# Optimization experiments

Hardware: AMD Instinct MI355X
Metric: run time of the kernel (lower is better)

The kernel has to match this reference:

```python
import jax, jax.numpy as jnp
import numpy as np

NUM_HEADS = 16


def setup_inputs() -> dict:
    key = jax.random.key(0)
    k1, k2, k3, k4 = jax.random.split(key, 4)
    B, S, E = 2, 2048, 1024
    x = jax.random.normal(k1, (B, S, E), dtype=jnp.float32)
    src_padding_mask = jax.random.randint(k2, (B, S), 0, 2) > 0  # True = keep
    # xavier-uniform-ish scale for linear weights (shape (out, in), torch convention)
    w_qkv = jax.random.normal(k3, (3 * E, E), dtype=jnp.float32) * (1.0 / np.sqrt(E))
    w_o = jax.random.normal(k4, (E, E), dtype=jnp.float32) * (1.0 / np.sqrt(E))
    return {"x": x, "src_padding_mask": src_padding_mask, "w_qkv": w_qkv, "w_o": w_o}


def reference(x, src_padding_mask, w_qkv, w_o):
    B, S, E = x.shape
    H = NUM_HEADS
    D = E // H
    # fused qkv projection: (B,S,3E) -> (B,S,H,3D) -> split
    qkv = jnp.einsum("bse,fe->bsf", x, w_qkv).reshape(B, S, H, 3 * D)
    q, k, v = jnp.split(qkv, 3, axis=-1)
    # (B,H,S,D)
    q = q.transpose(0, 2, 1, 3)
    k = k.transpose(0, 2, 1, 3)
    v = v.transpose(0, 2, 1, 3)
    logits = jnp.einsum("bhqd,bhkd->bhqk", q, k) / jnp.sqrt(jnp.float32(D))
    logits = jnp.where(src_padding_mask[:, None, None, :], logits, -jnp.inf)
    attn = jax.nn.softmax(logits, axis=-1)
    values = jnp.einsum("bhqk,bhkd->bhqd", attn, v)  # (B,H,S,D)
    values = values.transpose(0, 2, 1, 3).reshape(B, S, E)
    out = jnp.einsum("bse,fe->bsf", values, w_o)
    return out
```

## Files before the change

kernel.cpp:

```cpp
#include <hip/hip_runtime.h>
#include <hip/hip_bf16.h>

#define B_NUM 2
#define S_LEN 2048
#define E_DIM 1024
#define H_NUM 16
#define D_DIM 64
#define QKV_LD 3072
#define QSCALE_LOG2E 0.18033688011112042f

typedef __attribute__((ext_vector_type(8))) short bf16x8;
typedef __attribute__((ext_vector_type(8))) unsigned short u16x8;
typedef __attribute__((ext_vector_type(4))) unsigned short u16x4;
typedef __attribute__((ext_vector_type(4))) float f32x4;
typedef __attribute__((ext_vector_type(16))) float f32x16;
typedef __attribute__((ext_vector_type(2))) int i32x2;

static __device__ __forceinline__ unsigned short f2bf(float f) {
    union { float f; unsigned int u; } v; v.f = f;
    unsigned int r = v.u + 0x7fffu + ((v.u >> 16) & 1u);
    return (unsigned short)(r >> 16);
}

static __device__ __forceinline__ unsigned cvtpk_bf16(float lo, float hi) {
    unsigned r;
    asm("v_cvt_pk_bf16_f32 %0, %1, %2" : "=v"(r) : "v"(lo), "v"(hi));
    return r;
}

static __device__ __forceinline__ void gload16(const void* gsrc, void* ldst) {
    __builtin_amdgcn_global_load_lds(
        (const __attribute__((address_space(1))) unsigned int*)gsrc,
        (__attribute__((address_space(3))) unsigned int*)ldst, 16, 0, 0);
}

__global__ __launch_bounds__(256)
void cvt_f32_bf16(const float* __restrict__ in, unsigned short* __restrict__ outp, int n4) {
    int i = blockIdx.x * blockDim.x + threadIdx.x;
    if (i < n4) {
        float4 f = ((const float4*)in)[i];
        u16x4 o = { f2bf(f.x), f2bf(f.y), f2bf(f.z), f2bf(f.w) };
        ((u16x4*)outp)[i] = o;
    }
}

template <bool OUT_BF16, bool QSCALE>
__global__ __launch_bounds__(256)
void gemm_bt_mfma128(const unsigned short* __restrict__ A,
                     const unsigned short* __restrict__ Bw,
                     void* __restrict__ Cv, int M, int N, int K) {
    __shared__ unsigned short As[128 * 64];
    __shared__ unsigned short Bs[128 * 64];
    char* const AsB = (char*)As;
    char* const BsB = (char*)Bs;
    const int tid  = threadIdx.x;
    const int lane = tid & 63;
    const int w    = tid >> 6;
    const int lg   = lane >> 4;
    const int lq   = lane & 15;
    const int bm = blockIdx.y * 128;
    const int bn = blockIdx.x * 128;
    const int wr = (w >> 1) * 64;
    const int wc = (w & 1) * 64;
    const int lrow8 = lane >> 3;
    const int gblk  = (lane & 7) ^ lrow8;

    f32x4 acc[4][4];
#pragma unroll
    for (int i = 0; i < 4; ++i)
#pragma unroll
        for (int j = 0; j < 4; ++j) acc[i][j] = (f32x4){0.f, 0.f, 0.f, 0.f};

    for (int k0 = 0; k0 < K; k0 += 64) {
        __syncthreads();
#pragma unroll
        for (int t = 0; t < 4; ++t) {
            const int c = w * 4 + t;
            const int row = c * 8 + lrow8;
            gload16(A + (size_t)(bm + row) * K + k0 + gblk * 8, AsB + c * 1024);
            gload16(Bw + (size_t)(bn + row) * K + k0 + gblk * 8, BsB + c * 1024);
        }
        __syncthreads();

        bf16x8 af[4][2], bfr[4][2];
#pragma unroll
        for (int rt = 0; rt < 4; ++rt) {
            const int row = wr + rt * 16 + lq;
            const int sz = (row & 7) << 4;
            af[rt][0] = *(const bf16x8*)(AsB + row * 128 + ((lg * 16)      ^ sz));
            af[rt][1] = *(const bf16x8*)(AsB + row * 128 + ((64 + lg * 16) ^ sz));
        }
#pragma unroll
        for (int ct = 0; ct < 4; ++ct) {
            const int row = wc + ct * 16 + lq;
            const int sz = (row & 7) << 4;
            bfr[ct][0] = *(const bf16x8*)(BsB + row * 128 + ((lg * 16)      ^ sz));
            bfr[ct][1] = *(const bf16x8*)(BsB + row * 128 + ((64 + lg * 16) ^ sz));
        }
#pragma unroll
        for (int rt = 0; rt < 4; ++rt)
#pragma unroll
            for (int ct = 0; ct < 4; ++ct) {
                acc[rt][ct] = __builtin_amdgcn_mfma_f32_16x16x32_bf16(af[rt][0], bfr[ct][0], acc[rt][ct], 0, 0, 0);
                acc[rt][ct] = __builtin_amdgcn_mfma_f32_16x16x32_bf16(af[rt][1], bfr[ct][1], acc[rt][ct], 0, 0, 0);
            }
    }

#pragma unroll
    for (int rt = 0; rt < 4; ++rt)
#pragma unroll
        for (int ct = 0; ct < 4; ++ct) {
            const int row = bm + wr + rt * 16 + lg * 4;
            const int col = bn + wc + ct * 16 + lq;
            float scale = 1.f;
            if constexpr (QSCALE) scale = ((col % 192) < 64) ? QSCALE_LOG2E : 1.f;
#pragma unroll
            for (int r = 0; r < 4; ++r) {
                float vv = acc[rt][ct][r] * scale;
                if constexpr (OUT_BF16)
                    ((unsigned short*)Cv)[(size_t)(row + r) * N + col] = f2bf(vv);
                else
                    ((float*)Cv)[(size_t)(row + r) * N + col] = vv;
            }
        }
}

template <bool OUT_BF16, bool QSCALE>
__global__ __launch_bounds__(256)
void gemm_bt_mfma(const unsigned short* __restrict__ A,
                  const unsigned short* __restrict__ Bw,
                  void* __restrict__ Cv, int M, int N, int K) {
    __shared__ unsigned short As[64 * 64];
    __shared__ unsigned short Bs[64 * 64];
    char* const AsB = (char*)As;
    char* const BsB = (char*)Bs;
    const int tid  = threadIdx.x;
    const int lane = tid & 63;
    const int w    = tid >> 6;
    const int lg   = lane >> 4;
    const int lq   = lane & 15;
    const int bm = blockIdx.y * 64;
    const int bn = blockIdx.x * 64;
    const int wr = (w >> 1) * 32;
    const int wc = (w & 1) * 32;
    const int sr = tid >> 2;
    const int sc = (tid & 3) * 16;
    const int swzS = (sr & 7) << 4;

    f32x4 acc[2][2];
#pragma unroll
    for (int i = 0; i < 2; ++i)
#pragma unroll
        for (int j = 0; j < 2; ++j) acc[i][j] = (f32x4){0.f, 0.f, 0.f, 0.f};

    const unsigned short* ap = A  + (size_t)(bm + sr) * K + sc;
    const unsigned short* bp = Bw + (size_t)(bn + sr) * K + sc;

    for (int k0 = 0; k0 < K; k0 += 64) {
        __syncthreads();
        u16x8 av0 = *(const u16x8*)(ap + k0);
        u16x8 av1 = *(const u16x8*)(ap + k0 + 8);
        u16x8 bv0 = *(const u16x8*)(bp + k0);
        u16x8 bv1 = *(const u16x8*)(bp + k0 + 8);
        *(u16x8*)(AsB + sr * 128 + ((sc * 2)      ^ swzS)) = av0;
        *(u16x8*)(AsB + sr * 128 + ((sc * 2 + 16) ^ swzS)) = av1;
        *(u16x8*)(BsB + sr * 128 + ((sc * 2)      ^ swzS)) = bv0;
        *(u16x8*)(BsB + sr * 128 + ((sc * 2 + 16) ^ swzS)) = bv1;
        __syncthreads();

        bf16x8 af[2][2], bfr[2][2];
#pragma unroll
        for (int rt = 0; rt < 2; ++rt) {
            const int row = wr + rt * 16 + lq;
            const int sz = (row & 7) << 4;
            af[rt][0] = *(const bf16x8*)(AsB + row * 128 + ((lg * 16)      ^ sz));
            af[rt][1] = *(const bf16x8*)(AsB + row * 128 + ((64 + lg * 16) ^ sz));
        }
#pragma unroll
        for (int ct = 0; ct < 2; ++ct) {
            const int row = wc + ct * 16 + lq;
            const int sz = (row & 7) << 4;
            bfr[ct][0] = *(const bf16x8*)(BsB + row * 128 + ((lg * 16)      ^ sz));
            bfr[ct][1] = *(const bf16x8*)(BsB + row * 128 + ((64 + lg * 16) ^ sz));
        }
#pragma unroll
        for (int rt = 0; rt < 2; ++rt)
#pragma unroll
            for (int ct = 0; ct < 2; ++ct) {
                acc[rt][ct] = __builtin_amdgcn_mfma_f32_16x16x32_bf16(af[rt][0], bfr[ct][0], acc[rt][ct], 0, 0, 0);
                acc[rt][ct] = __builtin_amdgcn_mfma_f32_16x16x32_bf16(af[rt][1], bfr[ct][1], acc[rt][ct], 0, 0, 0);
            }
    }

#pragma unroll
    for (int rt = 0; rt < 2; ++rt)
#pragma unroll
        for (int ct = 0; ct < 2; ++ct) {
            const int row = bm + wr + rt * 16 + lg * 4;
            const int col = bn + wc + ct * 16 + lq;
            float scale = 1.f;
            if constexpr (QSCALE) scale = ((col % 192) < 64) ? QSCALE_LOG2E : 1.f;
#pragma unroll
            for (int r = 0; r < 4; ++r) {
                float vv = acc[rt][ct][r] * scale;
                if constexpr (OUT_BF16)
                    ((unsigned short*)Cv)[(size_t)(row + r) * N + col] = f2bf(vv);
                else
                    ((float*)Cv)[(size_t)(row + r) * N + col] = vv;
            }
        }
}

__global__ __launch_bounds__(256)
void attn_v6(const unsigned short* __restrict__ qkv, const int* __restrict__ mask,
             unsigned short* __restrict__ vout) {
    __shared__ __align__(16) char KsP[2][8192];
    __shared__ __align__(16) char VtP[2][8192];
    __shared__ __align__(16) float BiasF[S_LEN];

    const int tid  = threadIdx.x;
    const int lane = tid & 63;
    const int w    = tid >> 6;
    const int ln   = lane & 31;
    const int hi   = lane >> 5;
    const int q0 = blockIdx.x * 128;
    const int h  = blockIdx.y;
    const int b  = blockIdx.z;
    const size_t baseBH = (size_t)b * S_LEN * QKV_LD + (size_t)h * (3 * D_DIM);
    const unsigned short* const kv = qkv + baseBH;

    {
        const int4* mr = (const int4*)(mask + (size_t)b * S_LEN);
        int4 m0 = mr[tid * 2];
        int4 m1 = mr[tid * 2 + 1];
        float4 f0 = { m0.x ? 0.f : -30000.f, m0.y ? 0.f : -30000.f,
                      m0.z ? 0.f : -30000.f, m0.w ? 0.f : -30000.f };
        float4 f1 = { m1.x ? 0.f : -30000.f, m1.y ? 0.f : -30000.f,
                      m1.z ? 0.f : -30000.f, m1.w ? 0.f : -30000.f };
        ((float4*)BiasF)[tid * 2]     = f0;
        ((float4*)BiasF)[tid * 2 + 1] = f1;
    }

    bf16x8 qf[4];
    {
        const unsigned short* qp = kv + (size_t)(q0 + w * 32 + ln) * QKV_LD + hi * 8;
#pragma unroll
        for (int kk = 0; kk < 4; ++kk)
            qf[kk] = *(const bf16x8*)(qp + kk * 16);
    }

    const int lrow8 = lane >> 3;
    const int gblk  = (lane & 7) ^ lrow8;
    const int vkb = (tid & 15) * 4;
    const int vdb = (tid >> 4) * 4;

    {
#pragma unroll
        for (int t = 0; t < 2; ++t) {
            const int c = w * 2 + t;
            gload16(kv + (size_t)(c * 8 + lrow8) * QKV_LD + D_DIM + gblk * 8,
                    KsP[0] + c * 1024);
        }
        u16x4 vr[4];
#pragma unroll
        for (int i = 0; i < 4; ++i)
            vr[i] = *(const u16x4*)(kv + (size_t)(vkb + i) * QKV_LD + 2 * D_DIM + vdb);
#pragma unroll
        for (int j = 0; j < 4; ++j) {
            u16x4 o = { vr[0][j], vr[1][j], vr[2][j], vr[3][j] };
            const int row = vdb + j;
            *(u16x4*)(VtP[0] + row * 128 + ((vkb * 2) ^ ((row & 7) << 4))) = o;
        }
    }
    __syncthreads();

    f32x16 accO[2];
#pragma unroll
    for (int dt = 0; dt < 2; ++dt)
#pragma unroll
        for (int r = 0; r < 16; ++r) accO[dt][r] = 0.f;
    f32x4 rsumv = (f32x4){0.f, 0.f, 0.f, 0.f};

    for (int it = 0; it < S_LEN / 64; ++it) {
        const int cur = it & 1;
        const int kv0 = it * 64;
        char* const KsC = KsP[cur];
        char* const VtC = VtP[cur];
        const bool pf = (it < S_LEN / 64 - 1);

        u16x4 vr[4];
        if (pf) {
            const int kvn = kv0 + 64;
#pragma unroll
            for (int t = 0; t < 2; ++t) {
                const int c = w * 2 + t;
                gload16(kv + (size_t)(kvn + c * 8 + lrow8) * QKV_LD + D_DIM + gblk * 8,
                        KsP[cur ^ 1] + c * 1024);
            }
#pragma unroll
            for (int i = 0; i < 4; ++i)
                vr[i] = *(const u16x4*)(kv + (size_t)(kvn + vkb + i) * QKV_LD + 2 * D_DIM + vdb);
        }

        f32x16 s[2];
#pragma unroll
        for (int ks = 0; ks < 2; ++ks)
#pragma unroll
            for (int m = 0; m < 4; ++m) {
                f32x4 b4 = *(const f32x4*)(&BiasF[kv0 + ks * 32 + m * 8 + hi * 4]);
#pragma unroll
                for (int i = 0; i < 4; ++i) s[ks][m * 4 + i] = b4[i];
            }
        __builtin_amdgcn_s_setprio(1);
#pragma unroll
        for (int ks = 0; ks < 2; ++ks) {
            const int krow = ks * 32 + ln;
            const int swz = (ln & 7) << 4;
#pragma unroll
            for (int kk = 0; kk < 4; ++kk) {
                bf16x8 kf = *(const bf16x8*)(KsC + krow * 128 + (((kk * 16 + hi * 8) * 2) ^ swz));
                s[ks] = __builtin_amdgcn_mfma_f32_32x32x16_bf16(kf, qf[kk], s[ks], 0, 0, 0);
            }
        }
        __builtin_amdgcn_s_setprio(0);

#pragma unroll
        for (int ks = 0; ks < 2; ++ks)
#pragma unroll
            for (int r = 0; r < 16; ++r) {
                float p = __builtin_amdgcn_exp2f(s[ks][r]);
                s[ks][r] = p;
                rsumv[r & 3] += p;
            }

        bf16x8 pb[4];
#pragma unroll
        for (int ks = 0; ks < 2; ++ks) {
            unsigned wA[4], wB[4];
#pragma unroll
            for (int m = 0; m < 4; ++m) {
                wA[m] = cvtpk_bf16(s[ks][4 * m + 0], s[ks][4 * m + 1]);
                wB[m] = cvtpk_bf16(s[ks][4 * m + 2], s[ks][4 * m + 3]);
            }
#pragma unroll
            for (int t = 0; t < 2; ++t) {
                i32x2 ra = __builtin_amdgcn_permlane32_swap((int)wA[2 * t], (int)wA[2 * t + 1], false, false);
                i32x2 rb = __builtin_amdgcn_permlane32_swap((int)wB[2 * t], (int)wB[2 * t + 1], false, false);
                union { unsigned u[4]; bf16x8 v; } uu;
                uu.u[0] = (unsigned)ra[0];
                uu.u[1] = (unsigned)rb[0];
                uu.u[2] = (unsigned)ra[1];
                uu.u[3] = (unsigned)rb[1];
                pb[ks * 2 + t] = uu.v;
            }
        }

        __builtin_amdgcn_s_setprio(1);
#pragma unroll
        for (int dt = 0; dt < 2; ++dt) {
            const int drow = dt * 32 + ln;
            const int swz = (ln & 7) << 4;
#pragma unroll
            for (int n = 0; n < 4; ++n) {
                bf16x8 va = *(const bf16x8*)(VtC + drow * 128 + (((n * 16 + hi * 8) * 2) ^ swz));
                accO[dt] = __builtin_amdgcn_mfma_f32_32x32x16_bf16(va, pb[n], accO[dt], 0, 0, 0);
            }
        }
        __builtin_amdgcn_s_setprio(0);

        if (pf) {
#pragma unroll
            for (int j = 0; j < 4; ++j) {
                u16x4 o = { vr[0][j], vr[1][j], vr[2][j], vr[3][j] };
                const int row = vdb + j;
                *(u16x4*)(VtP[cur ^ 1] + row * 128 + ((vkb * 2) ^ ((row & 7) << 4))) = o;
            }
        }
        __syncthreads();
    }

    float rsum = rsumv[0] + rsumv[1] + rsumv[2] + rsumv[3];
    {
        i32x2 rr = __builtin_amdgcn_permlane32_swap(__float_as_int(rsum), __float_as_int(rsum), false, false);
        rsum = __int_as_float(rr[0]) + __int_as_float(rr[1]);
    }
    const float inv = 1.f / rsum;
    unsigned short* op = vout + (size_t)(b * S_LEN + q0 + w * 32 + ln) * E_DIM + h * D_DIM;
#pragma unroll
    for (int dt = 0; dt < 2; ++dt)
#pragma unroll
        for (int m = 0; m < 4; ++m) {
            u16x4 o;
#pragma unroll
            for (int i = 0; i < 4; ++i) o[i] = f2bf(accO[dt][4 * m + i] * inv);
            *(u16x4*)(op + dt * 32 + m * 8 + hi * 4) = o;
        }
}

extern "C" void kernel_launch(void* const* d_in, const int* in_sizes, int n_in,
                              void* d_out, int out_size, void* d_ws, size_t ws_size,
                              hipStream_t stream) {
    const float* x      = (const float*)d_in[0];
    const int*   mask   = (const int*)d_in[1];
    const float* w_qkv  = (const float*)d_in[2];
    const float* w_o    = (const float*)d_in[3];
    float*       out    = (float*)d_out;

    const int M = B_NUM * S_LEN;
    unsigned short* qkvb = (unsigned short*)d_ws;
    unsigned short* vbuf = qkvb + (size_t)M * 3 * E_DIM;
    unsigned short* xb   = vbuf + (size_t)M * E_DIM;
    unsigned short* wqb  = xb   + (size_t)M * E_DIM;
    unsigned short* wob  = wqb  + (size_t)3 * E_DIM * E_DIM;

    dim3 blk(256);
    {
        int n4;
        n4 = M * E_DIM / 4;
        cvt_f32_bf16<<<dim3((n4 + 255) / 256), blk, 0, stream>>>(x, xb, n4);
        n4 = 3 * E_DIM * E_DIM / 4;
        cvt_f32_bf16<<<dim3((n4 + 255) / 256), blk, 0, stream>>>(w_qkv, wqb, n4);
        n4 = E_DIM * E_DIM / 4;
        cvt_f32_bf16<<<dim3((n4 + 255) / 256), blk, 0, stream>>>(w_o, wob, n4);
    }

    gemm_bt_mfma128<true, true><<<dim3(3 * E_DIM / 128, M / 128), blk, 0, stream>>>(
        xb, wqb, qkvb, M, 3 * E_DIM, E_DIM);

    attn_v6<<<dim3(S_LEN / 128, H_NUM, B_NUM), blk, 0, stream>>>(qkvb, mask, vbuf);

    gemm_bt_mfma<false, false><<<dim3(E_DIM / 64, M / 64), blk, 0, stream>>>(
        vbuf, wob, out, M, E_DIM, E_DIM);
}
```

Baseline: 127.8 us.

## Triple-buffer K tiles in attention to prefetch two iterations ahead

The attention kernel gets a third K shared-memory buffer and issues the asynchronous K tile loads two iterations ahead, while V is still prefetched one iteration ahead. The per-iteration __syncthreads is replaced by an explicit lgkmcnt wait plus s_barrier that does not drain outstanding global loads, so K loads can stay in flight across the barrier. This aims to hide global-memory latency for K better. In exchange, LDS per block grows by 8 KB, which may reduce the number of resident blocks. Correctness now depends on in-order vmcnt completion, via the V register loads, to make each K tile visible before it is read.

```diff
diff --git a/kernel.cpp b/kernel.cpp
--- a/kernel.cpp
+++ b/kernel.cpp
@@ -212,9 +212,9 @@
 }
 
 __global__ __launch_bounds__(256)
-void attn_v6(const unsigned short* __restrict__ qkv, const int* __restrict__ mask,
+void attn_v7(const unsigned short* __restrict__ qkv, const int* __restrict__ mask,
              unsigned short* __restrict__ vout) {
-    __shared__ __align__(16) char KsP[2][8192];
+    __shared__ __align__(16) char KsP[3][8192];
     __shared__ __align__(16) char VtP[2][8192];
     __shared__ __align__(16) float BiasF[S_LEN];
 
@@ -260,6 +260,8 @@
             const int c = w * 2 + t;
             gload16(kv + (size_t)(c * 8 + lrow8) * QKV_LD + D_DIM + gblk * 8,
                     KsP[0] + c * 1024);
+            gload16(kv + (size_t)(64 + c * 8 + lrow8) * QKV_LD + D_DIM + gblk * 8,
+                    KsP[1] + c * 1024);
         }
         u16x4 vr[4];
 #pragma unroll
@@ -272,7 +274,10 @@
             *(u16x4*)(VtP[0] + row * 128 + ((vkb * 2) ^ ((row & 7) << 4))) = o;
         }
     }
-    __syncthreads();
+    __builtin_amdgcn_sched_barrier(0);
+    asm volatile("s_waitcnt vmcnt(0) lgkmcnt(0)" ::: "memory");
+    __builtin_amdgcn_s_barrier();
+    __builtin_amdgcn_sched_barrier(0);
 
     f32x16 accO[2];
 #pragma unroll
@@ -281,25 +286,32 @@
         for (int r = 0; r < 16; ++r) accO[dt][r] = 0.f;
     f32x4 rsumv = (f32x4){0.f, 0.f, 0.f, 0.f};
 
-    for (int it = 0; it < S_LEN / 64; ++it) {
-        const int cur = it & 1;
+    const int NT = S_LEN / 64;
+    int cur3 = 0;
+    int k2b  = 2;
+    for (int it = 0; it < NT; ++it) {
+        const int curv = it & 1;
         const int kv0 = it * 64;
-        char* const KsC = KsP[cur];
-        char* const VtC = VtP[cur];
-        const bool pf = (it < S_LEN / 64 - 1);
+        char* const KsC = KsP[cur3];
+        char* const VtC = VtP[curv];
+        const bool pfV = (it + 1 < NT);
+        const bool pfK = (it + 2 < NT);
 
         u16x4 vr[4];
-        if (pf) {
+        if (pfV) {
             const int kvn = kv0 + 64;
+#pragma unroll
+            for (int i = 0; i < 4; ++i)
+                vr[i] = *(const u16x4*)(kv + (size_t)(kvn + vkb + i) * QKV_LD + 2 * D_DIM + vdb);
+        }
+        if (pfK) {
+            const int kvn2 = kv0 + 128;
 #pragma unroll
             for (int t = 0; t < 2; ++t) {
                 const int c = w * 2 + t;
-                gload16(kv + (size_t)(kvn + c * 8 + lrow8) * QKV_LD + D_DIM + gblk * 8,
-                        KsP[cur ^ 1] + c * 1024);
-            }
-#pragma unroll
-            for (int i = 0; i < 4; ++i)
-                vr[i] = *(const u16x4*)(kv + (size_t)(kvn + vkb + i) * QKV_LD + 2 * D_DIM + vdb);
+                gload16(kv + (size_t)(kvn2 + c * 8 + lrow8) * QKV_LD + D_DIM + gblk * 8,
+                        KsP[k2b] + c * 1024);
+            }
         }
 
         f32x16 s[2];
@@ -368,15 +380,21 @@
         }
         __builtin_amdgcn_s_setprio(0);
 
-        if (pf) {
+        if (pfV) {
 #pragma unroll
             for (int j = 0; j < 4; ++j) {
                 u16x4 o = { vr[0][j], vr[1][j], vr[2][j], vr[3][j] };
                 const int row = vdb + j;
-                *(u16x4*)(VtP[cur ^ 1] + row * 128 + ((vkb * 2) ^ ((row & 7) << 4))) = o;
-            }
-        }
-        __syncthreads();
+                *(u16x4*)(VtP[curv ^ 1] + row * 128 + ((vkb * 2) ^ ((row & 7) << 4))) = o;
+            }
+            __builtin_amdgcn_sched_barrier(0);
+            asm volatile("s_waitcnt lgkmcnt(0)" ::: "memory");
+            __builtin_amdgcn_s_barrier();
+            __builtin_amdgcn_sched_barrier(0);
+        }
+
+        cur3 = (cur3 == 2) ? 0 : cur3 + 1;
+        k2b  = (k2b  == 2) ? 0 : k2b  + 1;
     }
 
     float rsum = rsumv[0] + rsumv[1] + rsumv[2] + rsumv[3];
@@ -427,7 +445,7 @@
     gemm_bt_mfma128<true, true><<<dim3(3 * E_DIM / 128, M / 128), blk, 0, stream>>>(
         xb, wqb, qkvb, M, 3 * E_DIM, E_DIM);
 
-    attn_v6<<<dim3(S_LEN / 128, H_NUM, B_NUM), blk, 0, stream>>>(qkvb, mask, vbuf);
+    attn_v7<<<dim3(S_LEN / 128, H_NUM, B_NUM), blk, 0, stream>>>(qkvb, mask, vbuf);
 
     gemm_bt_mfma<false, false><<<dim3(E_DIM / 64, M / 64), blk, 0, stream>>>(
         vbuf, wob, out, M, E_DIM, E_DIM);
```

Result: no change. 125.7 us (-1.6%).

## Split KV tile across warp pairs with 64-query warps and LDS partial-sum merge

Applied to the files above, without the earlier changes.

Each warp now handles 64 queries against half of every 64-key tile instead of 32 queries against the full tile. Each K fragment load then feeds two MFMAs, which cuts K LDS reads per MFMA. Warp pairs merge their partial outputs and row sums through shared memory at the end. Block indices are also remapped so that blocks sharing the same batch and head are spread across XCDs or are more co-resident. The price is more accumulator registers per warp and an extra reduction phase through LDS.

```diff
diff --git a/kernel.cpp b/kernel.cpp
--- a/kernel.cpp
+++ b/kernel.cpp
@@ -212,22 +212,30 @@
 }
 
 __global__ __launch_bounds__(256)
-void attn_v6(const unsigned short* __restrict__ qkv, const int* __restrict__ mask,
+void attn_v8(const unsigned short* __restrict__ qkv, const int* __restrict__ mask,
              unsigned short* __restrict__ vout) {
-    __shared__ __align__(16) char KsP[2][8192];
-    __shared__ __align__(16) char VtP[2][8192];
+    __shared__ __align__(16) char pool[32768];
     __shared__ __align__(16) float BiasF[S_LEN];
+    __shared__ float RsM[2][2][32];
 
     const int tid  = threadIdx.x;
     const int lane = tid & 63;
     const int w    = tid >> 6;
     const int ln   = lane & 31;
     const int hi   = lane >> 5;
-    const int q0 = blockIdx.x * 128;
-    const int h  = blockIdx.y;
-    const int b  = blockIdx.z;
-    const size_t baseBH = (size_t)b * S_LEN * QKV_LD + (size_t)h * (3 * D_DIM);
-    const unsigned short* const kv = qkv + baseBH;
+    const int qh   = w >> 1;
+    const int kh   = w & 1;
+
+    const int d0  = blockIdx.x + 16 * blockIdx.y + 256 * blockIdx.z;
+    const int lin = (d0 & 7) * 64 + (d0 >> 3);
+    const int q0 = (lin & 15) * 128;
+    const int h  = (lin >> 4) & 15;
+    const int b  = lin >> 8;
+    const unsigned short* const kv =
+        qkv + (size_t)b * S_LEN * QKV_LD + (size_t)h * (3 * D_DIM);
+
+    char* const poolK = pool;
+    char* const poolV = pool + 16384;
 
     {
         const int4* mr = (const int4*)(mask + (size_t)b * S_LEN);
@@ -241,12 +249,13 @@
         ((float4*)BiasF)[tid * 2 + 1] = f1;
     }
 
-    bf16x8 qf[4];
-    {
-        const unsigned short* qp = kv + (size_t)(q0 + w * 32 + ln) * QKV_LD + hi * 8;
+    bf16x8 qf[2][4];
+#pragma unroll
+    for (int qs = 0; qs < 2; ++qs) {
+        const unsigned short* qp = kv + (size_t)(q0 + qh * 64 + qs * 32 + ln) * QKV_LD + hi * 8;
 #pragma unroll
         for (int kk = 0; kk < 4; ++kk)
-            qf[kk] = *(const bf16x8*)(qp + kk * 16);
+            qf[qs][kk] = *(const bf16x8*)(qp + kk * 16);
     }
 
     const int lrow8 = lane >> 3;
@@ -259,7 +268,7 @@
         for (int t = 0; t < 2; ++t) {
             const int c = w * 2 + t;
             gload16(kv + (size_t)(c * 8 + lrow8) * QKV_LD + D_DIM + gblk * 8,
-                    KsP[0] + c * 1024);
+                    poolK + c * 1024);
         }
         u16x4 vr[4];
 #pragma unroll
@@ -269,24 +278,29 @@
         for (int j = 0; j < 4; ++j) {
             u16x4 o = { vr[0][j], vr[1][j], vr[2][j], vr[3][j] };
             const int row = vdb + j;
-            *(u16x4*)(VtP[0] + row * 128 + ((vkb * 2) ^ ((row & 7) << 4))) = o;
+            *(u16x4*)(poolV + row * 128 + ((vkb * 2) ^ ((row & 7) << 4))) = o;
         }
     }
     __syncthreads();
 
-    f32x16 accO[2];
+    f32x16 accO[2][2];
 #pragma unroll
     for (int dt = 0; dt < 2; ++dt)
 #pragma unroll
-        for (int r = 0; r < 16; ++r) accO[dt][r] = 0.f;
-    f32x4 rsumv = (f32x4){0.f, 0.f, 0.f, 0.f};
-
-    for (int it = 0; it < S_LEN / 64; ++it) {
+        for (int qs = 0; qs < 2; ++qs)
+#pragma unroll
+            for (int r = 0; r < 16; ++r) accO[dt][qs][r] = 0.f;
+    f32x4 rsv[2] = {(f32x4){0.f, 0.f, 0.f, 0.f}, (f32x4){0.f, 0.f, 0.f, 0.f}};
+
+    const int NT = S_LEN / 64;
+    const int krow = kh * 32 + ln;
+    const int kswz = (ln & 7) << 4;
+    for (int it = 0; it < NT; ++it) {
         const int cur = it & 1;
         const int kv0 = it * 64;
-        char* const KsC = KsP[cur];
-        char* const VtC = VtP[cur];
-        const bool pf = (it < S_LEN / 64 - 1);
+        char* const KsC = poolK + cur * 8192;
+        char* const VtC = poolV + cur * 8192;
+        const bool pf = (it + 1 < NT);
 
         u16x4 vr[4];
         if (pf) {
@@ -295,52 +309,51 @@
             for (int t = 0; t < 2; ++t) {
                 const int c = w * 2 + t;
                 gload16(kv + (size_t)(kvn + c * 8 + lrow8) * QKV_LD + D_DIM + gblk * 8,
-                        KsP[cur ^ 1] + c * 1024);
+                        poolK + (cur ^ 1) * 8192 + c * 1024);
             }
 #pragma unroll
             for (int i = 0; i < 4; ++i)
                 vr[i] = *(const u16x4*)(kv + (size_t)(kvn + vkb + i) * QKV_LD + 2 * D_DIM + vdb);
         }
 
+        bf16x8 kf[4];
+#pragma unroll
+        for (int kk = 0; kk < 4; ++kk)
+            kf[kk] = *(const bf16x8*)(KsC + krow * 128 + (((kk * 16 + hi * 8) * 2) ^ kswz));
+
         f32x16 s[2];
 #pragma unroll
-        for (int ks = 0; ks < 2; ++ks)
+        for (int m = 0; m < 4; ++m) {
+            f32x4 b4 = *(const f32x4*)(&BiasF[kv0 + kh * 32 + m * 8 + hi * 4]);
+#pragma unroll
+            for (int i = 0; i < 4; ++i) { s[0][m * 4 + i] = b4[i]; s[1][m * 4 + i] = b4[i]; }
+        }
+
+        __builtin_amdgcn_s_setprio(1);
+#pragma unroll
+        for (int kk = 0; kk < 4; ++kk) {
+            s[0] = __builtin_amdgcn_mfma_f32_32x32x16_bf16(kf[kk], qf[0][kk], s[0], 0, 0, 0);
+            s[1] = __builtin_amdgcn_mfma_f32_32x32x16_bf16(kf[kk], qf[1][kk], s[1], 0, 0, 0);
+        }
+        __builtin_amdgcn_s_setprio(0);
+
+#pragma unroll
+        for (int qs = 0; qs < 2; ++qs)
+#pragma unroll
+            for (int r = 0; r < 16; ++r) {
+                float p = __builtin_amdgcn_exp2f(s[qs][r]);
+                s[qs][r] = p;
+                rsv[qs][r & 3] += p;
+            }
+
+        bf16x8 pb[2][2];
+#pragma unroll
+        for (int qs = 0; qs < 2; ++qs) {
+            unsigned wA[4], wB[4];
 #pragma unroll
             for (int m = 0; m < 4; ++m) {
-                f32x4 b4 = *(const f32x4*)(&BiasF[kv0 + ks * 32 + m * 8 + hi * 4]);
-#pragma unroll
-                for (int i = 0; i < 4; ++i) s[ks][m * 4 + i] = b4[i];
-            }
-        __builtin_amdgcn_s_setprio(1);
-#pragma unroll
-        for (int ks = 0; ks < 2; ++ks) {
-            const int krow = ks * 32 + ln;
-            const int swz = (ln & 7) << 4;
-#pragma unroll
-            for (int kk = 0; kk < 4; ++kk) {
-                bf16x8 kf = *(const bf16x8*)(KsC + krow * 128 + (((kk * 16 + hi * 8) * 2) ^ swz));
-                s[ks] = __builtin_amdgcn_mfma_f32_32x32x16_bf16(kf, qf[kk], s[ks], 0, 0, 0);
-            }
-        }
-        __builtin_amdgcn_s_setprio(0);
-
-#pragma unroll
-        for (int ks = 0; ks < 2; ++ks)
-#pragma unroll
-            for (int r = 0; r < 16; ++r) {
-                float p = __builtin_amdgcn_exp2f(s[ks][r]);
-                s[ks][r] = p;
-                rsumv[r & 3] += p;
-            }
-
-        bf16x8 pb[4];
-#pragma unroll
-        for (int ks = 0; ks < 2; ++ks) {
-            unsigned wA[4], wB[4];
-#pragma unroll
-            for (int m = 0; m < 4; ++m) {
-                wA[m] = cvtpk_bf16(s[ks][4 * m + 0], s[ks][4 * m + 1]);
-                wB[m] = cvtpk_bf16(s[ks][4 * m + 2], s[ks][4 * m + 3]);
+                wA[m] = cvtpk_bf16(s[qs][4 * m + 0], s[qs][4 * m + 1]);
+                wB[m] = cvtpk_bf16(s[qs][4 * m + 2], s[qs][4 * m + 3]);
             }
 #pragma unroll
             for (int t = 0; t < 2; ++t) {
@@ -351,7 +364,7 @@
                 uu.u[1] = (unsigned)rb[0];
                 uu.u[2] = (unsigned)ra[1];
                 uu.u[3] = (unsigned)rb[1];
-                pb[ks * 2 + t] = uu.v;
+                pb[qs][t] = uu.v;
             }
         }
 
@@ -361,9 +374,11 @@
             const int drow = dt * 32 + ln;
             const int swz = (ln & 7) << 4;
 #pragma unroll
-            for (int n = 0; n < 4; ++n) {
+            for (int t = 0; t < 2; ++t) {
+                const int n = 2 * kh + t;
                 bf16x8 va = *(const bf16x8*)(VtC + drow * 128 + (((n * 16 + hi * 8) * 2) ^ swz));
-                accO[dt] = __builtin_amdgcn_mfma_f32_32x32x16_bf16(va, pb[n], accO[dt], 0, 0, 0);
+                accO[dt][0] = __builtin_amdgcn_mfma_f32_32x32x16_bf16(va, pb[0][t], accO[dt][0], 0, 0, 0);
+                accO[dt][1] = __builtin_amdgcn_mfma_f32_32x32x16_bf16(va, pb[1][t], accO[dt][1], 0, 0, 0);
             }
         }
         __builtin_amdgcn_s_setprio(0);
@@ -373,28 +388,58 @@
             for (int j = 0; j < 4; ++j) {
                 u16x4 o = { vr[0][j], vr[1][j], vr[2][j], vr[3][j] };
                 const int row = vdb + j;
-                *(u16x4*)(VtP[cur ^ 1] + row * 128 + ((vkb * 2) ^ ((row & 7) << 4))) = o;
+                *(u16x4*)(poolV + (cur ^ 1) * 8192 + row * 128 + ((vkb * 2) ^ ((row & 7) << 4))) = o;
             }
         }
         __syncthreads();
     }
 
-    float rsum = rsumv[0] + rsumv[1] + rsumv[2] + rsumv[3];
-    {
-        i32x2 rr = __builtin_amdgcn_permlane32_swap(__float_as_int(rsum), __float_as_int(rsum), false, false);
-        rsum = __int_as_float(rr[0]) + __int_as_float(rr[1]);
-    }
-    const float inv = 1.f / rsum;
-    unsigned short* op = vout + (size_t)(b * S_LEN + q0 + w * 32 + ln) * E_DIM + h * D_DIM;
-#pragma unroll
-    for (int dt = 0; dt < 2; ++dt)
-#pragma unroll
-        for (int m = 0; m < 4; ++m) {
-            u16x4 o;
-#pragma unroll
-            for (int i = 0; i < 4; ++i) o[i] = f2bf(accO[dt][4 * m + i] * inv);
-            *(u16x4*)(op + dt * 32 + m * 8 + hi * 4) = o;
-        }
+    float rs[2];
+#pragma unroll
+    for (int qs = 0; qs < 2; ++qs) {
+        float t = rsv[qs][0] + rsv[qs][1] + rsv[qs][2] + rsv[qs][3];
+        i32x2 rr = __builtin_amdgcn_permlane32_swap(__float_as_int(t), __float_as_int(t), false, false);
+        rs[qs] = __int_as_float(rr[0]) + __int_as_float(rr[1]);
+    }
+
+    __syncthreads();
+    const int lswz = (lane & 7) << 4;
+    if (kh == 1) {
+        char* const reg = pool + qh * 16384;
+#pragma unroll
+        for (int qs = 0; qs < 2; ++qs) {
+#pragma unroll
+            for (int dt = 0; dt < 2; ++dt)
+#pragma unroll
+                for (int r4 = 0; r4 < 4; ++r4) {
+                    f32x4 v = { accO[dt][qs][4 * r4 + 0], accO[dt][qs][4 * r4 + 1],
+                                accO[dt][qs][4 * r4 + 2], accO[dt][qs][4 * r4 + 3] };
+                    *(f32x4*)(reg + lane * 256 + ((qs * 128 + dt * 64 + r4 * 16) ^ lswz)) = v;
+                }
+            if (hi == 0) RsM[qh][qs][ln] = rs[qs];
+        }
+    }
+    __syncthreads();
+    if (kh == 0) {
+        const char* const reg = pool + qh * 16384;
+#pragma unroll
+        for (int qs = 0; qs < 2; ++qs) {
+            const float inv = 1.f / (rs[qs] + RsM[qh][qs][ln]);
+            unsigned short* op = vout +
+                (size_t)(b * S_LEN + q0 + qh * 64 + qs * 32 + ln) * E_DIM + h * D_DIM;
+#pragma unroll
+            for (int dt = 0; dt < 2; ++dt)
+#pragma unroll
+                for (int m = 0; m < 4; ++m) {
+                    f32x4 part = *(const f32x4*)(reg + lane * 256 + ((qs * 128 + dt * 64 + m * 16) ^ lswz));
+                    u16x4 o;
+#pragma unroll
+                    for (int i = 0; i < 4; ++i)
+                        o[i] = f2bf((accO[dt][qs][4 * m + i] + part[i]) * inv);
+                    *(u16x4*)(op + dt * 32 + m * 8 + hi * 4) = o;
+                }
+        }
+    }
 }
 
 extern "C" void kernel_launch(void* const* d_in, const int* in_sizes, int n_in,
@@ -427,7 +472,7 @@
     gemm_bt_mfma128<true, true><<<dim3(3 * E_DIM / 128, M / 128), blk, 0, stream>>>(
         xb, wqb, qkvb, M, 3 * E_DIM, E_DIM);
 
-    attn_v6<<<dim3(S_LEN / 128, H_NUM, B_NUM), blk, 0, stream>>>(qkvb, mask, vbuf);
+    attn_v8<<<dim3(S_LEN / 128, H_NUM, B_NUM), blk, 0, stream>>>(qkvb, mask, vbuf);
 
     gemm_bt_mfma<false, false><<<dim3(E_DIM / 64, M / 64), blk, 0, stream>>>(
         vbuf, wob, out, M, E_DIM, E_DIM);
```

Measured after the change: 129.3 us. No clear change (+1.2%).

## Split attention KV range into two halves and merge partial results

Applied to the files above, without the earlier changes.

The attention kernel now splits the 2048-key range into two 1024-key halves, so each (query tile, head, batch) gets two blocks and the grid doubles. Each half writes a normalized bf16 partial output and its row sum. A new merge kernel then combines the two partials, weighted by their row sums, into the head-interleaved value buffer. The goal is more concurrent blocks across the GPU's compute units. The cost is an extra kernel launch plus writing and re-reading the partial outputs. The partials are also rounded to bf16 before the merge, which adds a second rounding step.

```diff
diff --git a/kernel.cpp b/kernel.cpp
--- a/kernel.cpp
+++ b/kernel.cpp
@@ -20,6 +20,11 @@
     union { float f; unsigned int u; } v; v.f = f;
     unsigned int r = v.u + 0x7fffu + ((v.u >> 16) & 1u);
     return (unsigned short)(r >> 16);
+}
+
+static __device__ __forceinline__ float bf2f(unsigned short u) {
+    union { unsigned int u; float f; } v; v.u = ((unsigned int)u) << 16;
+    return v.f;
 }
 
 static __device__ __forceinline__ unsigned cvtpk_bf16(float lo, float hi) {
@@ -212,33 +217,31 @@
 }
 
 __global__ __launch_bounds__(256)
-void attn_v6(const unsigned short* __restrict__ qkv, const int* __restrict__ mask,
-             unsigned short* __restrict__ vout) {
+void attn_v14(const unsigned short* __restrict__ qkv, const int* __restrict__ mask,
+              unsigned short* __restrict__ Po, float* __restrict__ Zp) {
     __shared__ __align__(16) char KsP[2][8192];
     __shared__ __align__(16) char VtP[2][8192];
-    __shared__ __align__(16) float BiasF[S_LEN];
+    __shared__ __align__(16) float BiasF[1024];
 
     const int tid  = threadIdx.x;
     const int lane = tid & 63;
     const int w    = tid >> 6;
     const int ln   = lane & 31;
     const int hi   = lane >> 5;
-    const int q0 = blockIdx.x * 128;
+    const int part = blockIdx.x & 1;
+    const int q0   = (blockIdx.x >> 1) * 128;
     const int h  = blockIdx.y;
     const int b  = blockIdx.z;
-    const size_t baseBH = (size_t)b * S_LEN * QKV_LD + (size_t)h * (3 * D_DIM);
-    const unsigned short* const kv = qkv + baseBH;
+    const int kvbase = part * 1024;
+    const unsigned short* const kv =
+        qkv + (size_t)b * S_LEN * QKV_LD + (size_t)h * (3 * D_DIM);
 
     {
-        const int4* mr = (const int4*)(mask + (size_t)b * S_LEN);
-        int4 m0 = mr[tid * 2];
-        int4 m1 = mr[tid * 2 + 1];
+        const int4* mr = (const int4*)(mask + (size_t)b * S_LEN + kvbase);
+        int4 m0 = mr[tid];
         float4 f0 = { m0.x ? 0.f : -30000.f, m0.y ? 0.f : -30000.f,
                       m0.z ? 0.f : -30000.f, m0.w ? 0.f : -30000.f };
-        float4 f1 = { m1.x ? 0.f : -30000.f, m1.y ? 0.f : -30000.f,
-                      m1.z ? 0.f : -30000.f, m1.w ? 0.f : -30000.f };
-        ((float4*)BiasF)[tid * 2]     = f0;
-        ((float4*)BiasF)[tid * 2 + 1] = f1;
+        ((float4*)BiasF)[tid] = f0;
     }
 
     bf16x8 qf[4];
@@ -258,13 +261,13 @@
 #pragma unroll
         for (int t = 0; t < 2; ++t) {
             const int c = w * 2 + t;
-            gload16(kv + (size_t)(c * 8 + lrow8) * QKV_LD + D_DIM + gblk * 8,
+            gload16(kv + (size_t)(kvbase + c * 8 + lrow8) * QKV_LD + D_DIM + gblk * 8,
                     KsP[0] + c * 1024);
         }
         u16x4 vr[4];
 #pragma unroll
         for (int i = 0; i < 4; ++i)
-            vr[i] = *(const u16x4*)(kv + (size_t)(vkb + i) * QKV_LD + 2 * D_DIM + vdb);
+            vr[i] = *(const u16x4*)(kv + (size_t)(kvbase + vkb + i) * QKV_LD + 2 * D_DIM + vdb);
 #pragma unroll
         for (int j = 0; j < 4; ++j) {
             u16x4 o = { vr[0][j], vr[1][j], vr[2][j], vr[3][j] };
@@ -281,16 +284,18 @@
         for (int r = 0; r < 16; ++r) accO[dt][r] = 0.f;
     f32x4 rsumv = (f32x4){0.f, 0.f, 0.f, 0.f};
 
-    for (int it = 0; it < S_LEN / 64; ++it) {
+    const int NT = 16;
+    for (int it = 0; it < NT; ++it) {
         const int cur = it & 1;
-        const int kv0 = it * 64;
+        const int kv0l = it * 64;
+        const int kvg  = kvbase + it * 64;
         char* const KsC = KsP[cur];
         char* const VtC = VtP[cur];
-        const bool pf = (it < S_LEN / 64 - 1);
+        const bool pf = (it + 1 < NT);
 
         u16x4 vr[4];
         if (pf) {
-            const int kvn = kv0 + 64;
+            const int kvn = kvg + 64;
 #pragma unroll
             for (int t = 0; t < 2; ++t) {
                 const int c = w * 2 + t;
@@ -307,7 +312,7 @@
         for (int ks = 0; ks < 2; ++ks)
 #pragma unroll
             for (int m = 0; m < 4; ++m) {
-                f32x4 b4 = *(const f32x4*)(&BiasF[kv0 + ks * 32 + m * 8 + hi * 4]);
+                f32x4 b4 = *(const f32x4*)(&BiasF[kv0l + ks * 32 + m * 8 + hi * 4]);
 #pragma unroll
                 for (int i = 0; i < 4; ++i) s[ks][m * 4 + i] = b4[i];
             }
@@ -384,8 +389,9 @@
         i32x2 rr = __builtin_amdgcn_permlane32_swap(__float_as_int(rsum), __float_as_int(rsum), false, false);
         rsum = __int_as_float(rr[0]) + __int_as_float(rr[1]);
     }
+    const int q = q0 + w * 32 + ln;
     const float inv = 1.f / rsum;
-    unsigned short* op = vout + (size_t)(b * S_LEN + q0 + w * 32 + ln) * E_DIM + h * D_DIM;
+    unsigned short* po = Po + (((size_t)(part * B_NUM + b) * H_NUM + h) * S_LEN + q) * D_DIM;
 #pragma unroll
     for (int dt = 0; dt < 2; ++dt)
 #pragma unroll
@@ -393,8 +399,38 @@
             u16x4 o;
 #pragma unroll
             for (int i = 0; i < 4; ++i) o[i] = f2bf(accO[dt][4 * m + i] * inv);
-            *(u16x4*)(op + dt * 32 + m * 8 + hi * 4) = o;
-        }
+            *(u16x4*)(po + dt * 32 + m * 8 + hi * 4) = o;
+        }
+    if (hi == 0)
+        Zp[((size_t)(part * B_NUM + b) * H_NUM + h) * S_LEN + q] = rsum;
+}
+
+__global__ __launch_bounds__(256)
+void attn_merge(const unsigned short* __restrict__ Po, const float* __restrict__ Zp,
+                unsigned short* __restrict__ vbuf) {
+    const int idx = blockIdx.x * 256 + threadIdx.x;
+    const int j   = idx & 7;
+    const int rh  = idx >> 3;
+    const int h   = rh & (H_NUM - 1);
+    const int bq  = rh >> 4;
+    const int b   = bq >> 11;
+    const int q   = bq & (S_LEN - 1);
+
+    const size_t prow0 = ((size_t)(b)          * H_NUM + h) * S_LEN + q;
+    const size_t prow1 = ((size_t)(B_NUM + b)  * H_NUM + h) * S_LEN + q;
+    const float rs0 = Zp[prow0];
+    const float rs1 = Zp[prow1];
+    const float is = 1.f / (rs0 + rs1);
+    const float w0 = rs0 * is;
+    const float w1 = rs1 * is;
+
+    u16x8 a = *(const u16x8*)(Po + prow0 * D_DIM + j * 8);
+    u16x8 c = *(const u16x8*)(Po + prow1 * D_DIM + j * 8);
+    u16x8 o;
+#pragma unroll
+    for (int k = 0; k < 8; ++k)
+        o[k] = f2bf(bf2f(a[k]) * w0 + bf2f(c[k]) * w1);
+    *(u16x8*)(vbuf + (size_t)bq * E_DIM + h * D_DIM + j * 8) = o;
 }
 
 extern "C" void kernel_launch(void* const* d_in, const int* in_sizes, int n_in,
@@ -412,6 +448,8 @@
     unsigned short* xb   = vbuf + (size_t)M * E_DIM;
     unsigned short* wqb  = xb   + (size_t)M * E_DIM;
     unsigned short* wob  = wqb  + (size_t)3 * E_DIM * E_DIM;
+    unsigned short* Po   = wob  + (size_t)E_DIM * E_DIM;
+    float*          Zp   = (float*)(Po + (size_t)2 * M * E_DIM);
 
     dim3 blk(256);
     {
@@ -427,7 +465,10 @@
     gemm_bt_mfma128<true, true><<<dim3(3 * E_DIM / 128, M / 128), blk, 0, stream>>>(
         xb, wqb, qkvb, M, 3 * E_DIM, E_DIM);
 
-    attn_v6<<<dim3(S_LEN / 128, H_NUM, B_NUM), blk, 0, stream>>>(qkvb, mask, vbuf);
+    attn_v14<<<dim3((S_LEN / 128) * 2, H_NUM, B_NUM), blk, 0, stream>>>(
+        qkvb, mask, Po, Zp);
+
+    attn_merge<<<dim3(B_NUM * S_LEN * H_NUM * 8 / 256), blk, 0, stream>>>(Po, Zp, vbuf);
 
     gemm_bt_mfma<false, false><<<dim3(E_DIM / 64, M / 64), blk, 0, stream>>>(
         vbuf, wob, out, M, E_DIM, E_DIM);
```

Measured after the change: 134.7 us. 1.05x slower.
